# Kernel tuning notes

Hardware: AMD Instinct MI355X
Metric: run time of the kernel (lower is better)

## Reference

```python
import jax, jax.numpy as jnp
import numpy as np

N_NODES = 50000
N_EDGES = 800000
N_QUERY = 200000
EMBED = 128
HIDDEN = 128
N_CLASSES = 86


def setup_inputs() -> dict:
    key = jax.random.key(0)
    ks = jax.random.split(key, 12)
    x = jnp.arange(N_NODES, dtype=jnp.int64 if jax.config.jax_enable_x64 else jnp.int32)
    edge_index = jax.random.randint(ks[0], (2, N_EDGES), 0, N_NODES)
    edge_label_index = jax.random.randint(ks[1], (2, N_QUERY), 0, N_NODES)
    s_e = 1.0 / np.sqrt(EMBED)
    s_h = 1.0 / np.sqrt(HIDDEN)
    s_d = 1.0 / np.sqrt(2 * HIDDEN)
    emb = jax.random.normal(ks[2], (N_NODES, EMBED), jnp.float32)
    W1 = jax.random.uniform(ks[3], (EMBED, HIDDEN), jnp.float32, -s_e, s_e)
    b1 = jnp.zeros((HIDDEN,), jnp.float32)
    W2 = jax.random.uniform(ks[4], (HIDDEN, HIDDEN), jnp.float32, -s_h, s_h)
    b2 = jnp.zeros((HIDDEN,), jnp.float32)
    dW1 = jax.random.uniform(ks[5], (2 * HIDDEN, HIDDEN), jnp.float32, -s_d, s_d)
    db1 = jax.random.uniform(ks[6], (HIDDEN,), jnp.float32, -s_d, s_d)
    dW2 = jax.random.uniform(ks[7], (HIDDEN, N_CLASSES), jnp.float32, -s_h, s_h)
    db2 = jax.random.uniform(ks[8], (N_CLASSES,), jnp.float32, -s_h, s_h)
    return {"x": x, "edge_index": edge_index, "edge_label_index": edge_label_index,
            "emb": emb, "W1": W1, "b1": b1, "W2": W2, "b2": b2,
            "dW1": dW1, "db1": db1, "dW2": dW2, "db2": db2}


def gcn_conv(h, W, b, src, dst, n_nodes):
    """PyG-style GCNConv: linear, then D^-1/2 (A+I) D^-1/2 aggregation, then bias."""
    h = h @ W  # [N, H]
    # degree includes the implicit self-loop
    deg = jax.ops.segment_sum(jnp.ones_like(dst, dtype=h.dtype), dst, num_segments=n_nodes) + 1.0
    dis = jax.lax.rsqrt(deg)  # deg^{-1/2}
    norm = dis[src] * dis[dst]  # [E]
    msg = h[src] * norm[:, None]  # [E, H]
    agg = jax.ops.segment_sum(msg, dst, num_segments=n_nodes)
    agg = agg + h * (dis * dis)[:, None]  # self-loop messages
    return agg + b


def reference(x, edge_index, edge_label_index, emb, W1, b1, W2, b2, dW1, db1, dW2, db2):
    src, dst = edge_index[0], edge_index[1]
    h = emb[x]  # embedding lookup [N, E]
    h = gcn_conv(h, W1, b1, src, dst, N_NODES)
    h = jax.nn.relu(h)  # dropout is identity in eval mode
    z = gcn_conv(h, W2, b2, src, dst, N_NODES)
    # decode: gather pair endpoints, concat, 2-layer MLP
    feat = jnp.concatenate([z[edge_label_index[0]], z[edge_label_index[1]]], axis=-1)  # [Q, 2H]
    hdec = jax.nn.relu(feat @ dW1 + db1)
    logits = hdec @ dW2 + db2  # [Q, C]
    return logits
```

## Files before the change

### kernel.cpp

```cpp
#include <hip/hip_runtime.h>

#define NN 50000
#define NE 800000
#define NQ 200000
#define NC 86
#define CAP 64

typedef short short8 __attribute__((ext_vector_type(8)));
typedef float f32x4 __attribute__((ext_vector_type(4)));
typedef unsigned short us4 __attribute__((ext_vector_type(4)));

__device__ __forceinline__ unsigned short f2bf(float f) {
    unsigned u = __float_as_uint(f);
    u += 0x7FFF + ((u >> 16) & 1);
    return (unsigned short)(u >> 16);
}
__device__ __forceinline__ float bf_lo(unsigned p) { return __uint_as_float(p << 16); }
__device__ __forceinline__ float bf_hi(unsigned p) { return __uint_as_float(p & 0xffff0000u); }

__global__ __launch_bounds__(256) void k_fill(const int* __restrict__ src,
                                              const int* __restrict__ dst,
                                              int* __restrict__ cnt,
                                              unsigned short* __restrict__ slot) {
    int e = blockIdx.x * 256 + threadIdx.x;
    if (e >= NE) return;
    int d = dst[e];
    int p = atomicAdd(&cnt[d], 1);
    if (p < CAP) slot[(size_t)d * CAP + p] = (unsigned short)src[e];
}

__global__ __launch_bounds__(256) void k_dis(const int* __restrict__ cnt,
                                             float* __restrict__ dis) {
    int n = blockIdx.x * 256 + threadIdx.x;
    if (n < NN) dis[n] = rsqrtf((float)cnt[n] + 1.0f);
}

__global__ __launch_bounds__(256) void k_prep(const float* __restrict__ dW1,
                                              const float* __restrict__ dW2,
                                              unsigned short* __restrict__ W1t,
                                              unsigned short* __restrict__ W2t) {
    int i = blockIdx.x * 256 + threadIdx.x;
    if (i < 128 * 256) {
        int c = i >> 8, k = i & 255;
        W1t[c * 256 + k] = f2bf(dW1[k * 128 + c]);
    }
    if (i < 96 * 128) {
        int c = i >> 7, k = i & 127;
        W2t[c * 128 + k] = (c < NC) ? f2bf(dW2[k * NC + c]) : (unsigned short)0;
    }
}

template <bool GATHER, bool BF16IN>
__global__ __launch_bounds__(256) void k_linear(const void* __restrict__ Xv,
                                                const int* __restrict__ xidx,
                                                const float* __restrict__ W,
                                                unsigned short* __restrict__ out,
                                                int nrows) {
    __shared__ float Xl[64 * 128];
    const int t = threadIdx.x;
    const int r0 = blockIdx.x * 64;

    for (int i = t; i < 2048; i += 256) {
        int row = i >> 5, c4 = i & 31;
        int gr = r0 + row;
        float4 v = make_float4(0.f, 0.f, 0.f, 0.f);
        if (gr < nrows) {
            int sr = GATHER ? xidx[gr] : gr;
            if (BF16IN) {
                const unsigned* p = (const unsigned*)Xv + (size_t)sr * 64 + c4 * 2;
                unsigned u0 = p[0], u1 = p[1];
                v.x = bf_lo(u0); v.y = bf_hi(u0);
                v.z = bf_lo(u1); v.w = bf_hi(u1);
            } else {
                v = ((const float4*)((const float*)Xv + (size_t)sr * 128))[c4];
            }
        }
        ((float4*)Xl)[i] = v;
    }
    __syncthreads();

    const int tx = t & 31;
    const int ty = t >> 5;
    float4 acc[8];
#pragma unroll
    for (int q = 0; q < 8; ++q) acc[q] = make_float4(0.f, 0.f, 0.f, 0.f);

    const float* xr = Xl + ty * 8 * 128;
    for (int k = 0; k < 128; k += 4) {
        float4 w0 = ((const float4*)(W + (size_t)(k + 0) * 128))[tx];
        float4 w1 = ((const float4*)(W + (size_t)(k + 1) * 128))[tx];
        float4 w2 = ((const float4*)(W + (size_t)(k + 2) * 128))[tx];
        float4 w3 = ((const float4*)(W + (size_t)(k + 3) * 128))[tx];
#pragma unroll
        for (int q = 0; q < 8; ++q) {
            float4 xv = *((const float4*)(xr + q * 128 + k));
            acc[q].x = fmaf(xv.x, w0.x, acc[q].x); acc[q].y = fmaf(xv.x, w0.y, acc[q].y);
            acc[q].z = fmaf(xv.x, w0.z, acc[q].z); acc[q].w = fmaf(xv.x, w0.w, acc[q].w);
            acc[q].x = fmaf(xv.y, w1.x, acc[q].x); acc[q].y = fmaf(xv.y, w1.y, acc[q].y);
            acc[q].z = fmaf(xv.y, w1.z, acc[q].z); acc[q].w = fmaf(xv.y, w1.w, acc[q].w);
            acc[q].x = fmaf(xv.z, w2.x, acc[q].x); acc[q].y = fmaf(xv.z, w2.y, acc[q].y);
            acc[q].z = fmaf(xv.z, w2.z, acc[q].z); acc[q].w = fmaf(xv.z, w2.w, acc[q].w);
            acc[q].x = fmaf(xv.w, w3.x, acc[q].x); acc[q].y = fmaf(xv.w, w3.y, acc[q].y);
            acc[q].z = fmaf(xv.w, w3.z, acc[q].z); acc[q].w = fmaf(xv.w, w3.w, acc[q].w);
        }
    }

#pragma unroll
    for (int q = 0; q < 8; ++q) {
        int gr = r0 + ty * 8 + q;
        if (gr < nrows) {
            us4 o;
            o[0] = f2bf(acc[q].x); o[1] = f2bf(acc[q].y);
            o[2] = f2bf(acc[q].z); o[3] = f2bf(acc[q].w);
            *(us4*)(out + (size_t)gr * 128 + tx * 4) = o;
        }
    }
}

template <bool RELU>
__global__ __launch_bounds__(256) void k_agg(const int* __restrict__ cnt,
                                             const unsigned short* __restrict__ slot,
                                             const float* __restrict__ dis,
                                             const unsigned* __restrict__ hW,
                                             const float* __restrict__ b,
                                             unsigned* __restrict__ out) {
    int n = blockIdx.x * 4 + (threadIdx.x >> 6);
    int lane = threadIdx.x & 63;
    if (n >= NN) return;
    int c = cnt[n];
    if (c > CAP) c = CAP;
    float dn = dis[n];
    const unsigned short* sl = slot + (size_t)n * CAP;
    float a0 = 0.f, a1 = 0.f;
    int j = 0;
    for (; j + 3 < c; j += 4) {
        int s0 = sl[j], s1 = sl[j + 1], s2 = sl[j + 2], s3 = sl[j + 3];
        unsigned p0 = hW[(size_t)s0 * 64 + lane];
        unsigned p1 = hW[(size_t)s1 * 64 + lane];
        unsigned p2 = hW[(size_t)s2 * 64 + lane];
        unsigned p3 = hW[(size_t)s3 * 64 + lane];
        float nm0 = dn * dis[s0], nm1 = dn * dis[s1];
        float nm2 = dn * dis[s2], nm3 = dn * dis[s3];
        a0 = fmaf(bf_lo(p0), nm0, a0); a1 = fmaf(bf_hi(p0), nm0, a1);
        a0 = fmaf(bf_lo(p1), nm1, a0); a1 = fmaf(bf_hi(p1), nm1, a1);
        a0 = fmaf(bf_lo(p2), nm2, a0); a1 = fmaf(bf_hi(p2), nm2, a1);
        a0 = fmaf(bf_lo(p3), nm3, a0); a1 = fmaf(bf_hi(p3), nm3, a1);
    }
    for (; j < c; ++j) {
        int s0 = sl[j];
        unsigned p0 = hW[(size_t)s0 * 64 + lane];
        float nm0 = dn * dis[s0];
        a0 = fmaf(bf_lo(p0), nm0, a0); a1 = fmaf(bf_hi(p0), nm0, a1);
    }
    unsigned pn = hW[(size_t)n * 64 + lane];
    float r0 = fmaf(bf_lo(pn), dn * dn, a0) + b[2 * lane];
    float r1 = fmaf(bf_hi(pn), dn * dn, a1) + b[2 * lane + 1];
    if (RELU) {
        r0 = fmaxf(r0, 0.f);
        r1 = fmaxf(r1, 0.f);
    }
    out[(size_t)n * 64 + lane] = (unsigned)f2bf(r0) | ((unsigned)f2bf(r1) << 16);
}

__global__ __launch_bounds__(256) void k_decode(const int* __restrict__ eli,
                                                const unsigned short* __restrict__ z,
                                                const unsigned short* __restrict__ W1t,
                                                const float* __restrict__ db1,
                                                const unsigned short* __restrict__ W2t,
                                                const float* __restrict__ db2,
                                                float* __restrict__ out) {
    __shared__ short Fb[64 * 256];
    const int t = threadIdx.x;
    const int q0 = blockIdx.x * 64;
    const int lane = t & 63;
    const int w = t >> 6;
    const int lr = lane & 15;
    const int lk = lane >> 4;

#pragma unroll
    for (int it = 0; it < 8; ++it) {
        int g = it * 256 + t;
        int row = g >> 5, k8 = g & 31;
        int q = q0 + row;
        int node = (k8 < 16) ? eli[q] : eli[q + NQ];
        short8 v = *(const short8*)(z + (size_t)node * 128 + (k8 & 15) * 8);
        *(short8*)&Fb[row * 256 + (k8 ^ (row & 7)) * 8] = v;
    }
    __syncthreads();

    f32x4 acc[4][2];
#pragma unroll
    for (int i = 0; i < 4; ++i)
#pragma unroll
        for (int j = 0; j < 2; ++j) acc[i][j] = (f32x4){0.f, 0.f, 0.f, 0.f};

    for (int ks = 0; ks < 8; ++ks) {
        int k8 = ks * 4 + lk;
        short8 a[4];
#pragma unroll
        for (int rt = 0; rt < 4; ++rt) {
            int row = rt * 16 + lr;
            a[rt] = *(const short8*)&Fb[row * 256 + (k8 ^ (row & 7)) * 8];
        }
#pragma unroll
        for (int cc = 0; cc < 2; ++cc) {
            int col = (2 * w + cc) * 16 + lr;
            short8 b = *(const short8*)(W1t + col * 256 + ks * 32 + lk * 8);
#pragma unroll
            for (int rt = 0; rt < 4; ++rt)
                acc[rt][cc] = __builtin_amdgcn_mfma_f32_16x16x32_bf16(a[rt], b, acc[rt][cc], 0, 0, 0);
        }
    }
    __syncthreads();

#pragma unroll
    for (int cc = 0; cc < 2; ++cc) {
        int col = (2 * w + cc) * 16 + lr;
        float bv = db1[col];
#pragma unroll
        for (int rt = 0; rt < 4; ++rt) {
#pragma unroll
            for (int r = 0; r < 4; ++r) {
                int row = rt * 16 + lk * 4 + r;
                float hv = fmaxf(acc[rt][cc][r] + bv, 0.f);
                Fb[row * 128 + ((col >> 3) ^ (row & 7)) * 8 + (col & 7)] = (short)f2bf(hv);
            }
        }
    }
    __syncthreads();

    f32x4 acc2[6];
#pragma unroll
    for (int i = 0; i < 6; ++i) acc2[i] = (f32x4){0.f, 0.f, 0.f, 0.f};
    for (int ks = 0; ks < 4; ++ks) {
        int row = w * 16 + lr;
        int k8 = ks * 4 + lk;
        short8 a = *(const short8*)&Fb[row * 128 + (k8 ^ (row & 7)) * 8];
#pragma unroll
        for (int ct = 0; ct < 6; ++ct) {
            int col = ct * 16 + lr;
            short8 b = *(const short8*)(W2t + col * 128 + ks * 32 + lk * 8);
            acc2[ct] = __builtin_amdgcn_mfma_f32_16x16x32_bf16(a, b, acc2[ct], 0, 0, 0);
        }
    }
#pragma unroll
    for (int ct = 0; ct < 6; ++ct) {
        int c = ct * 16 + lr;
        if (c < NC) {
            float bv = db2[c];
#pragma unroll
            for (int r = 0; r < 4; ++r) {
                int q = q0 + w * 16 + lk * 4 + r;
                out[(size_t)q * NC + c] = acc2[ct][r] + bv;
            }
        }
    }
}

extern "C" void kernel_launch(void* const* d_in, const int* in_sizes, int n_in,
                              void* d_out, int out_size, void* d_ws, size_t ws_size,
                              hipStream_t stream) {
    const int* x = (const int*)d_in[0];
    const int* ei = (const int*)d_in[1];
    const int* eli = (const int*)d_in[2];
    const float* emb = (const float*)d_in[3];
    const float* W1 = (const float*)d_in[4];
    const float* b1 = (const float*)d_in[5];
    const float* W2 = (const float*)d_in[6];
    const float* b2 = (const float*)d_in[7];
    const float* dW1 = (const float*)d_in[8];
    const float* db1 = (const float*)d_in[9];
    const float* dW2 = (const float*)d_in[10];
    const float* db2 = (const float*)d_in[11];
    float* out = (float*)d_out;

    const int* src = ei;
    const int* dst = ei + NE;

    unsigned short* hA = (unsigned short*)d_ws;
    unsigned short* hB = hA + (size_t)NN * 128;
    int* cnt = (int*)(hB + (size_t)NN * 128);
    float* dis = (float*)(cnt + NN);
    unsigned short* slot = (unsigned short*)(dis + NN);
    unsigned short* W1t = slot + (size_t)NN * CAP;
    unsigned short* W2t = W1t + 128 * 256;

    hipMemsetAsync(cnt, 0, NN * sizeof(int), stream);
    k_prep<<<128, 256, 0, stream>>>(dW1, dW2, W1t, W2t);
    k_fill<<<(NE + 255) / 256, 256, 0, stream>>>(src, dst, cnt, slot);
    k_dis<<<(NN + 255) / 256, 256, 0, stream>>>(cnt, dis);

    k_linear<true, false><<<(NN + 63) / 64, 256, 0, stream>>>(emb, x, W1, hA, NN);
    k_agg<true><<<NN / 4, 256, 0, stream>>>(cnt, slot, dis, (const unsigned*)hA, b1,
                                            (unsigned*)hB);

    k_linear<false, true><<<(NN + 63) / 64, 256, 0, stream>>>(hB, nullptr, W2, hA, NN);
    k_agg<false><<<NN / 4, 256, 0, stream>>>(cnt, slot, dis, (const unsigned*)hA, b2,
                                             (unsigned*)hB);

    k_decode<<<NQ / 64, 256, 0, stream>>>(eli, hB, W1t, db1, W2t, db2, out);
}
```

Before: 371.8 us.

## Restructure decode to per-wave register tiles and unroll aggregation gather by eight

```diff
diff --git a/kernel.cpp b/kernel.cpp
--- a/kernel.cpp
+++ b/kernel.cpp
@@ -133,8 +133,35 @@
     const unsigned short* sl = slot + (size_t)n * CAP;
     float a0 = 0.f, a1 = 0.f;
     int j = 0;
+    for (; j + 7 < c; j += 8) {
+        us4 sa = *(const us4*)(sl + j);
+        us4 sb = *(const us4*)(sl + j + 4);
+        int s0 = sa[0], s1 = sa[1], s2 = sa[2], s3 = sa[3];
+        int s4 = sb[0], s5 = sb[1], s6 = sb[2], s7 = sb[3];
+        unsigned p0 = hW[(size_t)s0 * 64 + lane];
+        unsigned p1 = hW[(size_t)s1 * 64 + lane];
+        unsigned p2 = hW[(size_t)s2 * 64 + lane];
+        unsigned p3 = hW[(size_t)s3 * 64 + lane];
+        unsigned p4 = hW[(size_t)s4 * 64 + lane];
+        unsigned p5 = hW[(size_t)s5 * 64 + lane];
+        unsigned p6 = hW[(size_t)s6 * 64 + lane];
+        unsigned p7 = hW[(size_t)s7 * 64 + lane];
+        float nm0 = dn * dis[s0], nm1 = dn * dis[s1];
+        float nm2 = dn * dis[s2], nm3 = dn * dis[s3];
+        float nm4 = dn * dis[s4], nm5 = dn * dis[s5];
+        float nm6 = dn * dis[s6], nm7 = dn * dis[s7];
+        a0 = fmaf(bf_lo(p0), nm0, a0); a1 = fmaf(bf_hi(p0), nm0, a1);
+        a0 = fmaf(bf_lo(p1), nm1, a0); a1 = fmaf(bf_hi(p1), nm1, a1);
+        a0 = fmaf(bf_lo(p2), nm2, a0); a1 = fmaf(bf_hi(p2), nm2, a1);
+        a0 = fmaf(bf_lo(p3), nm3, a0); a1 = fmaf(bf_hi(p3), nm3, a1);
+        a0 = fmaf(bf_lo(p4), nm4, a0); a1 = fmaf(bf_hi(p4), nm4, a1);
+        a0 = fmaf(bf_lo(p5), nm5, a0); a1 = fmaf(bf_hi(p5), nm5, a1);
+        a0 = fmaf(bf_lo(p6), nm6, a0); a1 = fmaf(bf_hi(p6), nm6, a1);
+        a0 = fmaf(bf_lo(p7), nm7, a0); a1 = fmaf(bf_hi(p7), nm7, a1);
+    }
     for (; j + 3 < c; j += 4) {
-        int s0 = sl[j], s1 = sl[j + 1], s2 = sl[j + 2], s3 = sl[j + 3];
+        us4 sa = *(const us4*)(sl + j);
+        int s0 = sa[0], s1 = sa[1], s2 = sa[2], s3 = sa[3];
         unsigned p0 = hW[(size_t)s0 * 64 + lane];
         unsigned p1 = hW[(size_t)s1 * 64 + lane];
         unsigned p2 = hW[(size_t)s2 * 64 + lane];
@@ -169,90 +196,80 @@
                                                 const unsigned short* __restrict__ W2t,
                                                 const float* __restrict__ db2,
                                                 float* __restrict__ out) {
-    __shared__ short Fb[64 * 256];
+    __shared__ short Hs[4][16][128];
     const int t = threadIdx.x;
-    const int q0 = blockIdx.x * 64;
+    const int w = t >> 6;
     const int lane = t & 63;
-    const int w = t >> 6;
     const int lr = lane & 15;
     const int lk = lane >> 4;
-
-#pragma unroll
-    for (int it = 0; it < 8; ++it) {
-        int g = it * 256 + t;
-        int row = g >> 5, k8 = g & 31;
-        int q = q0 + row;
-        int node = (k8 < 16) ? eli[q] : eli[q + NQ];
-        short8 v = *(const short8*)(z + (size_t)node * 128 + (k8 & 15) * 8);
-        *(short8*)&Fb[row * 256 + (k8 ^ (row & 7)) * 8] = v;
-    }
-    __syncthreads();
-
-    f32x4 acc[4][2];
-#pragma unroll
-    for (int i = 0; i < 4; ++i)
-#pragma unroll
-        for (int j = 0; j < 2; ++j) acc[i][j] = (f32x4){0.f, 0.f, 0.f, 0.f};
-
+    const int qbase = blockIdx.x * 64 + w * 16;
+
+    const int u = eli[qbase + lr];
+    const int v = eli[qbase + lr + NQ];
+
+    short8 a[8];
+#pragma unroll
+    for (int ks = 0; ks < 8; ++ks) {
+        int node = (ks < 4) ? u : v;
+        int k8 = ks * 4 + lk;
+        a[ks] = *(const short8*)(z + (size_t)node * 128 + (k8 & 15) * 8);
+    }
+
+    f32x4 acc[8];
+#pragma unroll
+    for (int i = 0; i < 8; ++i) acc[i] = (f32x4){0.f, 0.f, 0.f, 0.f};
+#pragma unroll
     for (int ks = 0; ks < 8; ++ks) {
         int k8 = ks * 4 + lk;
-        short8 a[4];
-#pragma unroll
-        for (int rt = 0; rt < 4; ++rt) {
-            int row = rt * 16 + lr;
-            a[rt] = *(const short8*)&Fb[row * 256 + (k8 ^ (row & 7)) * 8];
-        }
-#pragma unroll
-        for (int cc = 0; cc < 2; ++cc) {
-            int col = (2 * w + cc) * 16 + lr;
-            short8 b = *(const short8*)(W1t + col * 256 + ks * 32 + lk * 8);
-#pragma unroll
-            for (int rt = 0; rt < 4; ++rt)
-                acc[rt][cc] = __builtin_amdgcn_mfma_f32_16x16x32_bf16(a[rt], b, acc[rt][cc], 0, 0, 0);
-        }
-    }
-    __syncthreads();
-
-#pragma unroll
-    for (int cc = 0; cc < 2; ++cc) {
-        int col = (2 * w + cc) * 16 + lr;
+#pragma unroll
+        for (int ct = 0; ct < 8; ++ct) {
+            int col = ct * 16 + lr;
+            short8 b = *(const short8*)(W1t + col * 256 + k8 * 8);
+            acc[ct] = __builtin_amdgcn_mfma_f32_16x16x32_bf16(a[ks], b, acc[ct], 0, 0, 0);
+        }
+    }
+
+#pragma unroll
+    for (int ct = 0; ct < 8; ++ct) {
+        int col = ct * 16 + lr;
         float bv = db1[col];
-#pragma unroll
-        for (int rt = 0; rt < 4; ++rt) {
-#pragma unroll
-            for (int r = 0; r < 4; ++r) {
-                int row = rt * 16 + lk * 4 + r;
-                float hv = fmaxf(acc[rt][cc][r] + bv, 0.f);
-                Fb[row * 128 + ((col >> 3) ^ (row & 7)) * 8 + (col & 7)] = (short)f2bf(hv);
-            }
-        }
-    }
-    __syncthreads();
+        int g = col >> 3, e = col & 7;
+#pragma unroll
+        for (int r = 0; r < 4; ++r) {
+            int row = lk * 4 + r;
+            float hv = fmaxf(acc[ct][r] + bv, 0.f);
+            Hs[w][row][(((g ^ row) & 15) << 3) + e] = (short)f2bf(hv);
+        }
+    }
 
     f32x4 acc2[6];
 #pragma unroll
     for (int i = 0; i < 6; ++i) acc2[i] = (f32x4){0.f, 0.f, 0.f, 0.f};
+#pragma unroll
     for (int ks = 0; ks < 4; ++ks) {
-        int row = w * 16 + lr;
         int k8 = ks * 4 + lk;
-        short8 a = *(const short8*)&Fb[row * 128 + (k8 ^ (row & 7)) * 8];
+        short8 hb = *(const short8*)&Hs[w][lr][((k8 ^ lr) & 15) << 3];
 #pragma unroll
         for (int ct = 0; ct < 6; ++ct) {
-            int col = ct * 16 + lr;
-            short8 b = *(const short8*)(W2t + col * 128 + ks * 32 + lk * 8);
-            acc2[ct] = __builtin_amdgcn_mfma_f32_16x16x32_bf16(a, b, acc2[ct], 0, 0, 0);
-        }
-    }
+            int cl = ct * 16 + lr;
+            short8 a2 = *(const short8*)(W2t + cl * 128 + k8 * 8);
+            acc2[ct] = __builtin_amdgcn_mfma_f32_16x16x32_bf16(a2, hb, acc2[ct], 0, 0, 0);
+        }
+    }
+
+    const int qq = qbase + lr;
+    float* orow = out + (size_t)qq * NC;
 #pragma unroll
     for (int ct = 0; ct < 6; ++ct) {
-        int c = ct * 16 + lr;
-        if (c < NC) {
-            float bv = db2[c];
-#pragma unroll
-            for (int r = 0; r < 4; ++r) {
-                int q = q0 + w * 16 + lk * 4 + r;
-                out[(size_t)q * NC + c] = acc2[ct][r] + bv;
-            }
+        int cbase = ct * 16 + lk * 4;
+        if (cbase + 3 < NC) {
+            float2 lo = {acc2[ct][0] + db2[cbase + 0], acc2[ct][1] + db2[cbase + 1]};
+            float2 hi = {acc2[ct][2] + db2[cbase + 2], acc2[ct][3] + db2[cbase + 3]};
+            *(float2*)(orow + cbase) = lo;
+            *(float2*)(orow + cbase + 2) = hi;
+        } else if (cbase < NC) {
+            float2 lo = {acc2[ct][0] + db2[84], acc2[ct][1] + db2[85]};
+            *(float2*)(orow + cbase) = lo;
         }
     }
 }
```

After: 429.7 us. +15.6%, slower.

## Unroll aggregation gather by 8 and prefetch second decode tile into registers

Applied to the files above, without the earlier changes.

```diff
diff --git a/kernel.cpp b/kernel.cpp
--- a/kernel.cpp
+++ b/kernel.cpp
@@ -133,8 +133,35 @@
     const unsigned short* sl = slot + (size_t)n * CAP;
     float a0 = 0.f, a1 = 0.f;
     int j = 0;
+    for (; j + 7 < c; j += 8) {
+        us4 sa = *(const us4*)(sl + j);
+        us4 sb = *(const us4*)(sl + j + 4);
+        int s0 = sa[0], s1 = sa[1], s2 = sa[2], s3 = sa[3];
+        int s4 = sb[0], s5 = sb[1], s6 = sb[2], s7 = sb[3];
+        unsigned p0 = hW[(size_t)s0 * 64 + lane];
+        unsigned p1 = hW[(size_t)s1 * 64 + lane];
+        unsigned p2 = hW[(size_t)s2 * 64 + lane];
+        unsigned p3 = hW[(size_t)s3 * 64 + lane];
+        unsigned p4 = hW[(size_t)s4 * 64 + lane];
+        unsigned p5 = hW[(size_t)s5 * 64 + lane];
+        unsigned p6 = hW[(size_t)s6 * 64 + lane];
+        unsigned p7 = hW[(size_t)s7 * 64 + lane];
+        float nm0 = dn * dis[s0], nm1 = dn * dis[s1];
+        float nm2 = dn * dis[s2], nm3 = dn * dis[s3];
+        float nm4 = dn * dis[s4], nm5 = dn * dis[s5];
+        float nm6 = dn * dis[s6], nm7 = dn * dis[s7];
+        a0 = fmaf(bf_lo(p0), nm0, a0); a1 = fmaf(bf_hi(p0), nm0, a1);
+        a0 = fmaf(bf_lo(p1), nm1, a0); a1 = fmaf(bf_hi(p1), nm1, a1);
+        a0 = fmaf(bf_lo(p2), nm2, a0); a1 = fmaf(bf_hi(p2), nm2, a1);
+        a0 = fmaf(bf_lo(p3), nm3, a0); a1 = fmaf(bf_hi(p3), nm3, a1);
+        a0 = fmaf(bf_lo(p4), nm4, a0); a1 = fmaf(bf_hi(p4), nm4, a1);
+        a0 = fmaf(bf_lo(p5), nm5, a0); a1 = fmaf(bf_hi(p5), nm5, a1);
+        a0 = fmaf(bf_lo(p6), nm6, a0); a1 = fmaf(bf_hi(p6), nm6, a1);
+        a0 = fmaf(bf_lo(p7), nm7, a0); a1 = fmaf(bf_hi(p7), nm7, a1);
+    }
     for (; j + 3 < c; j += 4) {
-        int s0 = sl[j], s1 = sl[j + 1], s2 = sl[j + 2], s3 = sl[j + 3];
+        us4 sa = *(const us4*)(sl + j);
+        int s0 = sa[0], s1 = sa[1], s2 = sa[2], s3 = sa[3];
         unsigned p0 = hW[(size_t)s0 * 64 + lane];
         unsigned p1 = hW[(size_t)s1 * 64 + lane];
         unsigned p2 = hW[(size_t)s2 * 64 + lane];
@@ -162,6 +189,81 @@
     out[(size_t)n * 64 + lane] = (unsigned)f2bf(r0) | ((unsigned)f2bf(r1) << 16);
 }
 
+__device__ __forceinline__ void decode_tile(short* Fb, int qt, int w, int lr, int lk,
+                                            const unsigned short* __restrict__ W1t,
+                                            const float* __restrict__ db1,
+                                            const unsigned short* __restrict__ W2t,
+                                            const float* __restrict__ db2,
+                                            float* __restrict__ out) {
+    f32x4 acc[4][2];
+#pragma unroll
+    for (int i = 0; i < 4; ++i)
+#pragma unroll
+        for (int j = 0; j < 2; ++j) acc[i][j] = (f32x4){0.f, 0.f, 0.f, 0.f};
+
+    for (int ks = 0; ks < 8; ++ks) {
+        int k8 = ks * 4 + lk;
+        short8 a[4];
+#pragma unroll
+        for (int rt = 0; rt < 4; ++rt) {
+            int row = rt * 16 + lr;
+            a[rt] = *(const short8*)&Fb[row * 256 + (k8 ^ (row & 7)) * 8];
+        }
+#pragma unroll
+        for (int cc = 0; cc < 2; ++cc) {
+            int col = (2 * w + cc) * 16 + lr;
+            short8 bfrag = *(const short8*)(W1t + col * 256 + ks * 32 + lk * 8);
+#pragma unroll
+            for (int rt = 0; rt < 4; ++rt)
+                acc[rt][cc] = __builtin_amdgcn_mfma_f32_16x16x32_bf16(a[rt], bfrag, acc[rt][cc], 0, 0, 0);
+        }
+    }
+    __syncthreads();
+
+#pragma unroll
+    for (int cc = 0; cc < 2; ++cc) {
+        int col = (2 * w + cc) * 16 + lr;
+        float bv = db1[col];
+#pragma unroll
+        for (int rt = 0; rt < 4; ++rt) {
+#pragma unroll
+            for (int r = 0; r < 4; ++r) {
+                int row = rt * 16 + lk * 4 + r;
+                float hv = fmaxf(acc[rt][cc][r] + bv, 0.f);
+                Fb[row * 128 + ((col >> 3) ^ (row & 7)) * 8 + (col & 7)] = (short)f2bf(hv);
+            }
+        }
+    }
+    __syncthreads();
+
+    f32x4 acc2[6];
+#pragma unroll
+    for (int i = 0; i < 6; ++i) acc2[i] = (f32x4){0.f, 0.f, 0.f, 0.f};
+    for (int ks = 0; ks < 4; ++ks) {
+        int row = w * 16 + lr;
+        int k8 = ks * 4 + lk;
+        short8 a = *(const short8*)&Fb[row * 128 + (k8 ^ (row & 7)) * 8];
+#pragma unroll
+        for (int ct = 0; ct < 6; ++ct) {
+            int col = ct * 16 + lr;
+            short8 bfrag = *(const short8*)(W2t + col * 128 + ks * 32 + lk * 8);
+            acc2[ct] = __builtin_amdgcn_mfma_f32_16x16x32_bf16(a, bfrag, acc2[ct], 0, 0, 0);
+        }
+    }
+#pragma unroll
+    for (int ct = 0; ct < 6; ++ct) {
+        int c = ct * 16 + lr;
+        if (c < NC) {
+            float bv = db2[c];
+#pragma unroll
+            for (int r = 0; r < 4; ++r) {
+                int q = qt + w * 16 + lk * 4 + r;
+                out[(size_t)q * NC + c] = acc2[ct][r] + bv;
+            }
+        }
+    }
+}
+
 __global__ __launch_bounds__(256) void k_decode(const int* __restrict__ eli,
                                                 const unsigned short* __restrict__ z,
                                                 const unsigned short* __restrict__ W1t,
@@ -171,11 +273,12 @@
                                                 float* __restrict__ out) {
     __shared__ short Fb[64 * 256];
     const int t = threadIdx.x;
-    const int q0 = blockIdx.x * 64;
+    const int w = t >> 6;
     const int lane = t & 63;
-    const int w = t >> 6;
     const int lr = lane & 15;
     const int lk = lane >> 4;
+    const int q0 = blockIdx.x * 128;
+    const bool has2 = (q0 + 64) < NQ;
 
 #pragma unroll
     for (int it = 0; it < 8; ++it) {
@@ -188,72 +291,30 @@
     }
     __syncthreads();
 
-    f32x4 acc[4][2];
-#pragma unroll
-    for (int i = 0; i < 4; ++i)
-#pragma unroll
-        for (int j = 0; j < 2; ++j) acc[i][j] = (f32x4){0.f, 0.f, 0.f, 0.f};
-
-    for (int ks = 0; ks < 8; ++ks) {
-        int k8 = ks * 4 + lk;
-        short8 a[4];
-#pragma unroll
-        for (int rt = 0; rt < 4; ++rt) {
-            int row = rt * 16 + lr;
-            a[rt] = *(const short8*)&Fb[row * 256 + (k8 ^ (row & 7)) * 8];
-        }
-#pragma unroll
-        for (int cc = 0; cc < 2; ++cc) {
-            int col = (2 * w + cc) * 16 + lr;
-            short8 b = *(const short8*)(W1t + col * 256 + ks * 32 + lk * 8);
-#pragma unroll
-            for (int rt = 0; rt < 4; ++rt)
-                acc[rt][cc] = __builtin_amdgcn_mfma_f32_16x16x32_bf16(a[rt], b, acc[rt][cc], 0, 0, 0);
-        }
-    }
-    __syncthreads();
-
-#pragma unroll
-    for (int cc = 0; cc < 2; ++cc) {
-        int col = (2 * w + cc) * 16 + lr;
-        float bv = db1[col];
-#pragma unroll
-        for (int rt = 0; rt < 4; ++rt) {
-#pragma unroll
-            for (int r = 0; r < 4; ++r) {
-                int row = rt * 16 + lk * 4 + r;
-                float hv = fmaxf(acc[rt][cc][r] + bv, 0.f);
-                Fb[row * 128 + ((col >> 3) ^ (row & 7)) * 8 + (col & 7)] = (short)f2bf(hv);
-            }
-        }
-    }
-    __syncthreads();
-
-    f32x4 acc2[6];
-#pragma unroll
-    for (int i = 0; i < 6; ++i) acc2[i] = (f32x4){0.f, 0.f, 0.f, 0.f};
-    for (int ks = 0; ks < 4; ++ks) {
-        int row = w * 16 + lr;
-        int k8 = ks * 4 + lk;
-        short8 a = *(const short8*)&Fb[row * 128 + (k8 ^ (row & 7)) * 8];
-#pragma unroll
-        for (int ct = 0; ct < 6; ++ct) {
-            int col = ct * 16 + lr;
-            short8 b = *(const short8*)(W2t + col * 128 + ks * 32 + lk * 8);
-            acc2[ct] = __builtin_amdgcn_mfma_f32_16x16x32_bf16(a, b, acc2[ct], 0, 0, 0);
-        }
-    }
-#pragma unroll
-    for (int ct = 0; ct < 6; ++ct) {
-        int c = ct * 16 + lr;
-        if (c < NC) {
-            float bv = db2[c];
-#pragma unroll
-            for (int r = 0; r < 4; ++r) {
-                int q = q0 + w * 16 + lk * 4 + r;
-                out[(size_t)q * NC + c] = acc2[ct][r] + bv;
-            }
-        }
+    short8 pre[8];
+    if (has2) {
+#pragma unroll
+        for (int it = 0; it < 8; ++it) {
+            int g = it * 256 + t;
+            int row = g >> 5, k8 = g & 31;
+            int q = q0 + 64 + row;
+            int node = (k8 < 16) ? eli[q] : eli[q + NQ];
+            pre[it] = *(const short8*)(z + (size_t)node * 128 + (k8 & 15) * 8);
+        }
+    }
+
+    decode_tile(Fb, q0, w, lr, lk, W1t, db1, W2t, db2, out);
+
+    if (has2) {
+        __syncthreads();
+#pragma unroll
+        for (int it = 0; it < 8; ++it) {
+            int g = it * 256 + t;
+            int row = g >> 5, k8 = g & 31;
+            *(short8*)&Fb[row * 256 + (k8 ^ (row & 7)) * 8] = pre[it];
+        }
+        __syncthreads();
+        decode_tile(Fb, q0 + 64, w, lr, lk, W1t, db1, W2t, db2, out);
     }
 }
 
@@ -298,5 +359,5 @@
     k_agg<false><<<NN / 4, 256, 0, stream>>>(cnt, slot, dis, (const unsigned*)hA, b2,
                                              (unsigned*)hB);
 
-    k_decode<<<NQ / 64, 256, 0, stream>>>(eli, hB, W1t, db1, W2t, db2, out);
-}
+    k_decode<<<(NQ / 64 + 1) / 2, 256, 0, stream>>>(eli, hB, W1t, db1, W2t, db2, out);
+}
```

After: 373.7 us. About the same (+0.5%).

## Use bf16 MFMA for GCN linear layers and vectorize neighbor aggregation

Applied to the files above, without the earlier changes.

```diff
diff --git a/kernel.cpp b/kernel.cpp
--- a/kernel.cpp
+++ b/kernel.cpp
@@ -37,8 +37,12 @@
 
 __global__ __launch_bounds__(256) void k_prep(const float* __restrict__ dW1,
                                               const float* __restrict__ dW2,
+                                              const float* __restrict__ W1,
+                                              const float* __restrict__ W2,
                                               unsigned short* __restrict__ W1t,
-                                              unsigned short* __restrict__ W2t) {
+                                              unsigned short* __restrict__ W2t,
+                                              unsigned short* __restrict__ W1c,
+                                              unsigned short* __restrict__ W2c) {
     int i = blockIdx.x * 256 + threadIdx.x;
     if (i < 128 * 256) {
         int c = i >> 8, k = i & 255;
@@ -48,71 +52,75 @@
         int c = i >> 7, k = i & 127;
         W2t[c * 128 + k] = (c < NC) ? f2bf(dW2[k * NC + c]) : (unsigned short)0;
     }
+    if (i < 128 * 128) {
+        int c = i >> 7, k = i & 127;
+        W1c[c * 128 + k] = f2bf(W1[k * 128 + c]);
+        W2c[c * 128 + k] = f2bf(W2[k * 128 + c]);
+    }
 }
 
 template <bool GATHER, bool BF16IN>
 __global__ __launch_bounds__(256) void k_linear(const void* __restrict__ Xv,
                                                 const int* __restrict__ xidx,
-                                                const float* __restrict__ W,
+                                                const unsigned short* __restrict__ Wt,
                                                 unsigned short* __restrict__ out,
                                                 int nrows) {
-    __shared__ float Xl[64 * 128];
+    __shared__ short Xb[64 * 128];
     const int t = threadIdx.x;
     const int r0 = blockIdx.x * 64;
 
-    for (int i = t; i < 2048; i += 256) {
-        int row = i >> 5, c4 = i & 31;
-        int gr = r0 + row;
-        float4 v = make_float4(0.f, 0.f, 0.f, 0.f);
-        if (gr < nrows) {
-            int sr = GATHER ? xidx[gr] : gr;
+#pragma unroll
+    for (int it = 0; it < 4; ++it) {
+        int g = it * 256 + t;
+        int row = g >> 4, g8 = g & 15;
+        int node = r0 + row;
+        short8 v = (short8){0, 0, 0, 0, 0, 0, 0, 0};
+        if (node < nrows) {
+            int sr = GATHER ? xidx[node] : node;
             if (BF16IN) {
-                const unsigned* p = (const unsigned*)Xv + (size_t)sr * 64 + c4 * 2;
-                unsigned u0 = p[0], u1 = p[1];
-                v.x = bf_lo(u0); v.y = bf_hi(u0);
-                v.z = bf_lo(u1); v.w = bf_hi(u1);
+                v = *(const short8*)((const unsigned short*)Xv + (size_t)sr * 128 + g8 * 8);
             } else {
-                v = ((const float4*)((const float*)Xv + (size_t)sr * 128))[c4];
+                const float* p = (const float*)Xv + (size_t)sr * 128 + g8 * 8;
+                float4 f0 = ((const float4*)p)[0];
+                float4 f1 = ((const float4*)p)[1];
+                v[0] = (short)f2bf(f0.x); v[1] = (short)f2bf(f0.y);
+                v[2] = (short)f2bf(f0.z); v[3] = (short)f2bf(f0.w);
+                v[4] = (short)f2bf(f1.x); v[5] = (short)f2bf(f1.y);
+                v[6] = (short)f2bf(f1.z); v[7] = (short)f2bf(f1.w);
             }
         }
-        ((float4*)Xl)[i] = v;
+        *(short8*)&Xb[row * 128 + ((g8 ^ (row & 7)) * 8)] = v;
     }
     __syncthreads();
 
-    const int tx = t & 31;
-    const int ty = t >> 5;
-    float4 acc[8];
-#pragma unroll
-    for (int q = 0; q < 8; ++q) acc[q] = make_float4(0.f, 0.f, 0.f, 0.f);
-
-    const float* xr = Xl + ty * 8 * 128;
-    for (int k = 0; k < 128; k += 4) {
-        float4 w0 = ((const float4*)(W + (size_t)(k + 0) * 128))[tx];
-        float4 w1 = ((const float4*)(W + (size_t)(k + 1) * 128))[tx];
-        float4 w2 = ((const float4*)(W + (size_t)(k + 2) * 128))[tx];
-        float4 w3 = ((const float4*)(W + (size_t)(k + 3) * 128))[tx];
-#pragma unroll
-        for (int q = 0; q < 8; ++q) {
-            float4 xv = *((const float4*)(xr + q * 128 + k));
-            acc[q].x = fmaf(xv.x, w0.x, acc[q].x); acc[q].y = fmaf(xv.x, w0.y, acc[q].y);
-            acc[q].z = fmaf(xv.x, w0.z, acc[q].z); acc[q].w = fmaf(xv.x, w0.w, acc[q].w);
-            acc[q].x = fmaf(xv.y, w1.x, acc[q].x); acc[q].y = fmaf(xv.y, w1.y, acc[q].y);
-            acc[q].z = fmaf(xv.y, w1.z, acc[q].z); acc[q].w = fmaf(xv.y, w1.w, acc[q].w);
-            acc[q].x = fmaf(xv.z, w2.x, acc[q].x); acc[q].y = fmaf(xv.z, w2.y, acc[q].y);
-            acc[q].z = fmaf(xv.z, w2.z, acc[q].z); acc[q].w = fmaf(xv.z, w2.w, acc[q].w);
-            acc[q].x = fmaf(xv.w, w3.x, acc[q].x); acc[q].y = fmaf(xv.w, w3.y, acc[q].y);
-            acc[q].z = fmaf(xv.w, w3.z, acc[q].z); acc[q].w = fmaf(xv.w, w3.w, acc[q].w);
-        }
-    }
-
-#pragma unroll
-    for (int q = 0; q < 8; ++q) {
-        int gr = r0 + ty * 8 + q;
-        if (gr < nrows) {
+    const int w = t >> 6;
+    const int lane = t & 63;
+    const int lr = lane & 15;
+    const int lk = lane >> 4;
+    const int qrow = w * 16 + lr;
+
+    f32x4 acc[8];
+#pragma unroll
+    for (int i = 0; i < 8; ++i) acc[i] = (f32x4){0.f, 0.f, 0.f, 0.f};
+
+    for (int ks = 0; ks < 4; ++ks) {
+        int k8 = ks * 4 + lk;
+        short8 b = *(const short8*)&Xb[qrow * 128 + ((k8 ^ (qrow & 7)) * 8)];
+#pragma unroll
+        for (int ct = 0; ct < 8; ++ct) {
+            short8 a = *(const short8*)(Wt + (size_t)(ct * 16 + lr) * 128 + k8 * 8);
+            acc[ct] = __builtin_amdgcn_mfma_f32_16x16x32_bf16(a, b, acc[ct], 0, 0, 0);
+        }
+    }
+
+    int q = r0 + w * 16 + lr;
+    if (q < nrows) {
+#pragma unroll
+        for (int ct = 0; ct < 8; ++ct) {
             us4 o;
-            o[0] = f2bf(acc[q].x); o[1] = f2bf(acc[q].y);
-            o[2] = f2bf(acc[q].z); o[3] = f2bf(acc[q].w);
-            *(us4*)(out + (size_t)gr * 128 + tx * 4) = o;
+            o[0] = f2bf(acc[ct][0]); o[1] = f2bf(acc[ct][1]);
+            o[2] = f2bf(acc[ct][2]); o[3] = f2bf(acc[ct][3]);
+            *(us4*)(out + (size_t)q * 128 + ct * 16 + lk * 4) = o;
         }
     }
 }
@@ -126,40 +134,61 @@
                                              unsigned* __restrict__ out) {
     int n = blockIdx.x * 4 + (threadIdx.x >> 6);
     int lane = threadIdx.x & 63;
+    int half = lane >> 5, li = lane & 31;
     if (n >= NN) return;
     int c = cnt[n];
     if (c > CAP) c = CAP;
     float dn = dis[n];
-    const unsigned short* sl = slot + (size_t)n * CAP;
-    float a0 = 0.f, a1 = 0.f;
-    int j = 0;
-    for (; j + 3 < c; j += 4) {
-        int s0 = sl[j], s1 = sl[j + 1], s2 = sl[j + 2], s3 = sl[j + 3];
-        unsigned p0 = hW[(size_t)s0 * 64 + lane];
-        unsigned p1 = hW[(size_t)s1 * 64 + lane];
-        unsigned p2 = hW[(size_t)s2 * 64 + lane];
-        unsigned p3 = hW[(size_t)s3 * 64 + lane];
-        float nm0 = dn * dis[s0], nm1 = dn * dis[s1];
-        float nm2 = dn * dis[s2], nm3 = dn * dis[s3];
-        a0 = fmaf(bf_lo(p0), nm0, a0); a1 = fmaf(bf_hi(p0), nm0, a1);
-        a0 = fmaf(bf_lo(p1), nm1, a0); a1 = fmaf(bf_hi(p1), nm1, a1);
-        a0 = fmaf(bf_lo(p2), nm2, a0); a1 = fmaf(bf_hi(p2), nm2, a1);
-        a0 = fmaf(bf_lo(p3), nm3, a0); a1 = fmaf(bf_hi(p3), nm3, a1);
-    }
-    for (; j < c; ++j) {
-        int s0 = sl[j];
-        unsigned p0 = hW[(size_t)s0 * 64 + lane];
-        float nm0 = dn * dis[s0];
-        a0 = fmaf(bf_lo(p0), nm0, a0); a1 = fmaf(bf_hi(p0), nm0, a1);
-    }
-    unsigned pn = hW[(size_t)n * 64 + lane];
-    float r0 = fmaf(bf_lo(pn), dn * dn, a0) + b[2 * lane];
-    float r1 = fmaf(bf_hi(pn), dn * dn, a1) + b[2 * lane + 1];
-    if (RELU) {
-        r0 = fmaxf(r0, 0.f);
-        r1 = fmaxf(r1, 0.f);
-    }
-    out[(size_t)n * 64 + lane] = (unsigned)f2bf(r0) | ((unsigned)f2bf(r1) << 16);
+    int sv = slot[(size_t)n * CAP + lane];
+
+    float a0 = 0.f, a1 = 0.f, a2 = 0.f, a3 = 0.f;
+    for (int j = 0; j < c; j += 16) {
+        int s[8];
+        float nm[8];
+#pragma unroll
+        for (int k = 0; k < 8; ++k) {
+            int e = j + 2 * k + half;
+            int sk = __shfl(sv, e & 63);
+            bool ok = e < c;
+            s[k] = ok ? sk : 0;
+            nm[k] = ok ? 1.0f : 0.0f;
+        }
+        uint2 p[8];
+#pragma unroll
+        for (int k = 0; k < 8; ++k)
+            p[k] = *(const uint2*)(hW + (size_t)s[k] * 64 + 2 * li);
+#pragma unroll
+        for (int k = 0; k < 8; ++k) nm[k] *= dn * dis[s[k]];
+#pragma unroll
+        for (int k = 0; k < 8; ++k) {
+            a0 = fmaf(bf_lo(p[k].x), nm[k], a0);
+            a1 = fmaf(bf_hi(p[k].x), nm[k], a1);
+            a2 = fmaf(bf_lo(p[k].y), nm[k], a2);
+            a3 = fmaf(bf_hi(p[k].y), nm[k], a3);
+        }
+    }
+    a0 += __shfl_xor(a0, 32);
+    a1 += __shfl_xor(a1, 32);
+    a2 += __shfl_xor(a2, 32);
+    a3 += __shfl_xor(a3, 32);
+
+    if (half == 0) {
+        uint2 pn = *(const uint2*)(hW + (size_t)n * 64 + 2 * li);
+        float d2 = dn * dn;
+        float4 bb = *(const float4*)(b + 4 * li);
+        float r0 = fmaf(bf_lo(pn.x), d2, a0) + bb.x;
+        float r1 = fmaf(bf_hi(pn.x), d2, a1) + bb.y;
+        float r2 = fmaf(bf_lo(pn.y), d2, a2) + bb.z;
+        float r3 = fmaf(bf_hi(pn.y), d2, a3) + bb.w;
+        if (RELU) {
+            r0 = fmaxf(r0, 0.f); r1 = fmaxf(r1, 0.f);
+            r2 = fmaxf(r2, 0.f); r3 = fmaxf(r3, 0.f);
+        }
+        uint2 o;
+        o.x = (unsigned)f2bf(r0) | ((unsigned)f2bf(r1) << 16);
+        o.y = (unsigned)f2bf(r2) | ((unsigned)f2bf(r3) << 16);
+        *(uint2*)(out + (size_t)n * 64 + 2 * li) = o;
+    }
 }
 
 __global__ __launch_bounds__(256) void k_decode(const int* __restrict__ eli,
@@ -205,10 +234,10 @@
 #pragma unroll
         for (int cc = 0; cc < 2; ++cc) {
             int col = (2 * w + cc) * 16 + lr;
-            short8 b = *(const short8*)(W1t + col * 256 + ks * 32 + lk * 8);
+            short8 bfrag = *(const short8*)(W1t + col * 256 + ks * 32 + lk * 8);
 #pragma unroll
             for (int rt = 0; rt < 4; ++rt)
-                acc[rt][cc] = __builtin_amdgcn_mfma_f32_16x16x32_bf16(a[rt], b, acc[rt][cc], 0, 0, 0);
+                acc[rt][cc] = __builtin_amdgcn_mfma_f32_16x16x32_bf16(a[rt], bfrag, acc[rt][cc], 0, 0, 0);
         }
     }
     __syncthreads();
@@ -239,8 +268,8 @@
 #pragma unroll
         for (int ct = 0; ct < 6; ++ct) {
             int col = ct * 16 + lr;
-            short8 b = *(const short8*)(W2t + col * 128 + ks * 32 + lk * 8);
-            acc2[ct] = __builtin_amdgcn_mfma_f32_16x16x32_bf16(a, b, acc2[ct], 0, 0, 0);
+            short8 bfrag = *(const short8*)(W2t + col * 128 + ks * 32 + lk * 8);
+            acc2[ct] = __builtin_amdgcn_mfma_f32_16x16x32_bf16(a, bfrag, acc2[ct], 0, 0, 0);
         }
     }
 #pragma unroll
@@ -282,19 +311,21 @@
     int* cnt = (int*)(hB + (size_t)NN * 128);
     float* dis = (float*)(cnt + NN);
     unsigned short* slot = (unsigned short*)(dis + NN);
-    unsigned short* W1t = slot + (size_t)NN * CAP;
+    unsigned short* W1t = slot + (size_t)NN * CAP + 64;
     unsigned short* W2t = W1t + 128 * 256;
+    unsigned short* W1c = W2t + 96 * 128;
+    unsigned short* W2c = W1c + 128 * 128;
 
     hipMemsetAsync(cnt, 0, NN * sizeof(int), stream);
-    k_prep<<<128, 256, 0, stream>>>(dW1, dW2, W1t, W2t);
+    k_prep<<<128, 256, 0, stream>>>(dW1, dW2, W1, W2, W1t, W2t, W1c, W2c);
     k_fill<<<(NE + 255) / 256, 256, 0, stream>>>(src, dst, cnt, slot);
     k_dis<<<(NN + 255) / 256, 256, 0, stream>>>(cnt, dis);
 
-    k_linear<true, false><<<(NN + 63) / 64, 256, 0, stream>>>(emb, x, W1, hA, NN);
+    k_linear<true, false><<<(NN + 63) / 64, 256, 0, stream>>>(emb, x, W1c, hA, NN);
     k_agg<true><<<NN / 4, 256, 0, stream>>>(cnt, slot, dis, (const unsigned*)hA, b1,
                                             (unsigned*)hB);
 
-    k_linear<false, true><<<(NN + 63) / 64, 256, 0, stream>>>(hB, nullptr, W2, hA, NN);
+    k_linear<false, true><<<(NN + 63) / 64, 256, 0, stream>>>(hB, nullptr, W2c, hA, NN);
     k_agg<false><<<NN / 4, 256, 0, stream>>>(cnt, slot, dis, (const unsigned*)hA, b2,
                                              (unsigned*)hB);
 
```

After: 365.8 us. About the same (-1.6%).
